# Kernel tuning notes

Hardware: AMD Instinct MI355X
Metric: run time of the kernel (lower is better)

Reference implementation:

```python
import jax, jax.numpy as jnp
import numpy as np

HEADS = 8
DIM_HEAD = 64
DIM_INNER = HEADS * DIM_HEAD  # 512
SCALE = DIM_HEAD ** -0.5
B, N, D = 8, 512, 512
NEG = -1e9


def setup_inputs() -> dict:
    key = jax.random.key(0)
    ks = jax.random.split(key, 12)
    inp = {}
    for i in range(3):
        inp[f"x{i}"] = jax.random.normal(ks[i], (B, N, D), dtype=jnp.float32)
        inp[f"m{i}"] = jax.random.randint(ks[3 + i], (B, N), 0, 2).astype(bool)
        inp[f"Wqkv{i}"] = jax.random.normal(ks[6 + i], (D, 3 * DIM_INNER), dtype=jnp.float32) * 0.02
        inp[f"Wout{i}"] = jax.random.normal(ks[9 + i], (DIM_INNER, D), dtype=jnp.float32) * 0.02
    return inp


def _split_heads(t):
    # [b, n, h*d] -> [b, h, n, d]
    b, n, _ = t.shape
    return t.reshape(b, n, HEADS, DIM_HEAD).transpose(0, 2, 1, 3)


def _forward(xs, masks, Wqkvs, Wouts):
    qs, ks, vs = [], [], []
    for x, W in zip(xs, Wqkvs):
        q, k, v = jnp.split(x @ W, 3, axis=-1)
        qs.append(_split_heads(q))
        ks.append(_split_heads(k))
        vs.append(_split_heads(v))
    K = jnp.concatenate(ks, axis=2)  # [b, h, 3n, d]
    V = jnp.concatenate(vs, axis=2)
    outs = []
    for q, m, Wo in zip(qs, masks, Wouts):
        dots = jnp.einsum('bhnd,bhmd->bhnm', q, K) * SCALE
        # original masks whole query rows: masked_fill(~mask[:, None, :, None], -1e9)
        dots = jnp.where(m[:, None, :, None], dots, NEG)
        attn = jax.nn.softmax(dots, axis=-1)  # dropout is identity at eval
        o = jnp.einsum('bhnm,bhmd->bhnd', attn, V)
        o = o.transpose(0, 2, 1, 3).reshape(q.shape[0], q.shape[2], DIM_INNER)
        outs.append(o @ Wo)
    return tuple(outs)


def reference(x0, x1, x2, m0, m1, m2, Wqkv0, Wqkv1, Wqkv2, Wout0, Wout1, Wout2):
    return _forward((x0, x1, x2), (m0, m1, m2), (Wqkv0, Wqkv1, Wqkv2), (Wout0, Wout1, Wout2))
```

## Files before the change

### kernel.cpp

```cpp
#include <hip/hip_runtime.h>
#include <cstdint>
#include <cstddef>

#define NEGV  -1.0e9f
#define QSCALE 0.18033688011112042f

typedef _Float16 h8 __attribute__((ext_vector_type(8)));
typedef _Float16 h4 __attribute__((ext_vector_type(4)));
typedef float    f4 __attribute__((ext_vector_type(4)));


__global__ __launch_bounds__(256) void cvt_x(
    const float* __restrict__ x0, const float* __restrict__ x1, const float* __restrict__ x2,
    _Float16* __restrict__ xh)
{
    const int mod = blockIdx.y;
    const float* __restrict__ s = (mod == 0) ? x0 : ((mod == 1) ? x1 : x2);
    _Float16* __restrict__ d = xh + (size_t)mod * 2097152;
    const int i = (blockIdx.x * 256 + threadIdx.x) * 4;
    float4 v = *reinterpret_cast<const float4*>(&s[i]);
    h4 o = { (_Float16)v.x, (_Float16)v.y, (_Float16)v.z, (_Float16)v.w };
    *reinterpret_cast<h4*>(&d[i]) = o;
}

__global__ __launch_bounds__(256) void tr_cvt(
    const float* __restrict__ s0, const float* __restrict__ s1, const float* __restrict__ s2,
    _Float16* __restrict__ dst, int R, int C)
{
    const int mod = blockIdx.z;
    const float* __restrict__ s = (mod == 0) ? s0 : ((mod == 1) ? s1 : s2);
    _Float16* __restrict__ d = dst + (size_t)mod * R * C;
    const int c0 = blockIdx.x * 32, r0 = blockIdx.y * 32;
    __shared__ float tile[32][33];
    const int tr = threadIdx.x >> 3;
    const int tc = (threadIdx.x & 7) * 4;
    float4 v = *reinterpret_cast<const float4*>(&s[(size_t)(r0 + tr) * C + c0 + tc]);
    tile[tr][tc + 0] = v.x; tile[tr][tc + 1] = v.y; tile[tr][tc + 2] = v.z; tile[tr][tc + 3] = v.w;
    __syncthreads();
    h4 o = { (_Float16)tile[tc + 0][tr], (_Float16)tile[tc + 1][tr],
             (_Float16)tile[tc + 2][tr], (_Float16)tile[tc + 3][tr] };
    *reinterpret_cast<h4*>(&d[(size_t)(c0 + tr) * R + r0 + tc]) = o;
}

__global__ __launch_bounds__(256) void qkv_gemm_f16(
    const _Float16* __restrict__ xh, const _Float16* __restrict__ Wqt,
    _Float16* __restrict__ Qh, _Float16* __restrict__ Kh, _Float16* __restrict__ Vt)
{
    const int mod = blockIdx.z;
    const _Float16* __restrict__ A  = xh  + (size_t)mod * 4096 * 512;
    const _Float16* __restrict__ Bw = Wqt + (size_t)mod * 1536 * 512;

    __shared__ _Float16 As[128 * 40];
    __shared__ _Float16 Bs[128 * 40];

    const int t = threadIdx.x;
    const int brow = blockIdx.y * 128, bcol = blockIdx.x * 128;
    const int w = t >> 6, l = t & 63;
    const int wr = (w >> 1) * 64, wc = (w & 1) * 64;
    const int lr = l & 15, lk = (l >> 4) * 8, lg = l >> 4;

    const int sm0 = t >> 2,        skk = (t & 3) * 8;
    const int sm1 = (t + 256) >> 2;

    f4 acc[4][4] = {};
    h8 arg[2], brg[2];

    arg[0] = *reinterpret_cast<const h8*>(&A [(size_t)(brow + sm0) * 512 + skk]);
    arg[1] = *reinterpret_cast<const h8*>(&A [(size_t)(brow + sm1) * 512 + skk]);
    brg[0] = *reinterpret_cast<const h8*>(&Bw[(size_t)(bcol + sm0) * 512 + skk]);
    brg[1] = *reinterpret_cast<const h8*>(&Bw[(size_t)(bcol + sm1) * 512 + skk]);
    *reinterpret_cast<h8*>(&As[sm0 * 40 + skk]) = arg[0];
    *reinterpret_cast<h8*>(&As[sm1 * 40 + skk]) = arg[1];
    *reinterpret_cast<h8*>(&Bs[sm0 * 40 + skk]) = brg[0];
    *reinterpret_cast<h8*>(&Bs[sm1 * 40 + skk]) = brg[1];

    for (int k0 = 0; k0 < 512; k0 += 32) {
        __syncthreads();
        const bool more = (k0 + 32) < 512;
        if (more) {
            const int kn = k0 + 32;
            arg[0] = *reinterpret_cast<const h8*>(&A [(size_t)(brow + sm0) * 512 + kn + skk]);
            arg[1] = *reinterpret_cast<const h8*>(&A [(size_t)(brow + sm1) * 512 + kn + skk]);
            brg[0] = *reinterpret_cast<const h8*>(&Bw[(size_t)(bcol + sm0) * 512 + kn + skk]);
            brg[1] = *reinterpret_cast<const h8*>(&Bw[(size_t)(bcol + sm1) * 512 + kn + skk]);
        }
        h8 af[4], bf[4];
#pragma unroll
        for (int m = 0; m < 4; m++)
            af[m] = *reinterpret_cast<h8*>(&As[(wr + m * 16 + lr) * 40 + lk]);
#pragma unroll
        for (int n = 0; n < 4; n++)
            bf[n] = *reinterpret_cast<h8*>(&Bs[(wc + n * 16 + lr) * 40 + lk]);
        __builtin_amdgcn_s_setprio(1);
#pragma unroll
        for (int m = 0; m < 4; m++)
#pragma unroll
            for (int n = 0; n < 4; n++)
                acc[m][n] = __builtin_amdgcn_mfma_f32_16x16x32_f16(af[m], bf[n], acc[m][n], 0, 0, 0);
        __builtin_amdgcn_s_setprio(0);
        __syncthreads();
        if (more) {
            *reinterpret_cast<h8*>(&As[sm0 * 40 + skk]) = arg[0];
            *reinterpret_cast<h8*>(&As[sm1 * 40 + skk]) = arg[1];
            *reinterpret_cast<h8*>(&Bs[sm0 * 40 + skk]) = brg[0];
            *reinterpret_cast<h8*>(&Bs[sm1 * 40 + skk]) = brg[1];
        }
    }

    const int sec = bcol >> 9;
    const int b = brow >> 9;
    const int nbase = brow & 511;
    const int cbase = bcol - (sec << 9);

#pragma unroll
    for (int m = 0; m < 4; m++) {
        const int rloc = wr + m * 16 + lg * 4;
#pragma unroll
        for (int reg = 0; reg < 4; reg++) {
            const int n = nbase + rloc + reg;
#pragma unroll
            for (int nn = 0; nn < 4; nn++) {
                const int cis = cbase + wc + nn * 16 + lr;
                const int h = cis >> 6, d = cis & 63;
                const float v = acc[m][nn][reg];
                if (sec == 0) {
                    Qh[((((size_t)mod * 8 + b) * 8 + h) * 512 + n) * 64 + d] = (_Float16)(v * QSCALE);
                } else if (sec == 1) {
                    Kh[(((size_t)b * 8 + h) * 1536 + mod * 512 + n) * 64 + d] = (_Float16)v;
                } else {
                    Vt[(((size_t)b * 8 + h) * 64 + d) * 1536 + mod * 512 + n] = (_Float16)v;
                }
            }
        }
    }
}

__global__ __launch_bounds__(256) void attn_f16(
    const _Float16* __restrict__ Qh, const _Float16* __restrict__ Kh, const _Float16* __restrict__ Vt,
    const int* __restrict__ m0, const int* __restrict__ m1, const int* __restrict__ m2,
    _Float16* __restrict__ Oh)
{
    const int mod = blockIdx.z;
    const int bh = blockIdx.y, b = bh >> 3, h = bh & 7;
    const int q0 = blockIdx.x * 64;

    __shared__ _Float16 Ks[64 * 72];
    __shared__ _Float16 Vs[64 * 72];
    __shared__ _Float16 Ps[64 * 72];

    const int t = threadIdx.x, w = t >> 6, l = t & 63;
    const int lr = l & 15, lg = l >> 4, lk = lg * 8;

    const _Float16* __restrict__ Qp = Qh + ((((size_t)mod * 8 + b) * 8 + h) * 512 + q0 + w * 16) * 64;
    h8 qf0 = *reinterpret_cast<const h8*>(&Qp[(size_t)lr * 64 + lk]);
    h8 qf1 = *reinterpret_cast<const h8*>(&Qp[(size_t)lr * 64 + 32 + lk]);

    const int* __restrict__ mk = (mod == 0) ? m0 : ((mod == 1) ? m1 : m2);
    const bool msk = mk[b * 512 + q0 + w * 16 + lr] != 0;

    float mrow = -3.0e38f, lsum = 0.f;
    f4 o[4] = {};

    const _Float16* __restrict__ Kp = Kh + (size_t)bh * 1536 * 64;
    const _Float16* __restrict__ Vp = Vt + (size_t)bh * 64 * 1536;

    const int sr0 = t >> 3,        skk = (t & 7) * 8;
    const int sr1 = (t + 256) >> 3;

    h8 krg[2], vrg[2];
    krg[0] = *reinterpret_cast<const h8*>(&Kp[(size_t)sr0 * 64 + skk]);
    krg[1] = *reinterpret_cast<const h8*>(&Kp[(size_t)sr1 * 64 + skk]);
    vrg[0] = *reinterpret_cast<const h8*>(&Vp[(size_t)sr0 * 1536 + skk]);
    vrg[1] = *reinterpret_cast<const h8*>(&Vp[(size_t)sr1 * 1536 + skk]);
    *reinterpret_cast<h8*>(&Ks[sr0 * 72 + skk]) = krg[0];
    *reinterpret_cast<h8*>(&Ks[sr1 * 72 + skk]) = krg[1];
    *reinterpret_cast<h8*>(&Vs[sr0 * 72 + skk]) = vrg[0];
    *reinterpret_cast<h8*>(&Vs[sr1 * 72 + skk]) = vrg[1];

    for (int c0 = 0; c0 < 1536; c0 += 64) {
        __syncthreads();
        const bool more = (c0 + 64) < 1536;
        if (more) {
            const int cn = c0 + 64;
            krg[0] = *reinterpret_cast<const h8*>(&Kp[(size_t)(cn + sr0) * 64 + skk]);
            krg[1] = *reinterpret_cast<const h8*>(&Kp[(size_t)(cn + sr1) * 64 + skk]);
            vrg[0] = *reinterpret_cast<const h8*>(&Vp[(size_t)sr0 * 1536 + cn + skk]);
            vrg[1] = *reinterpret_cast<const h8*>(&Vp[(size_t)sr1 * 1536 + cn + skk]);
        }

        f4 st[4] = {};
        __builtin_amdgcn_s_setprio(1);
#pragma unroll
        for (int kb = 0; kb < 4; kb++) {
            h8 ka0 = *reinterpret_cast<h8*>(&Ks[(kb * 16 + lr) * 72 + lk]);
            h8 ka1 = *reinterpret_cast<h8*>(&Ks[(kb * 16 + lr) * 72 + 32 + lk]);
            st[kb] = __builtin_amdgcn_mfma_f32_16x16x32_f16(ka0, qf0, st[kb], 0, 0, 0);
            st[kb] = __builtin_amdgcn_mfma_f32_16x16x32_f16(ka1, qf1, st[kb], 0, 0, 0);
        }
        __builtin_amdgcn_s_setprio(0);

        if (!msk) {
#pragma unroll
            for (int kb = 0; kb < 4; kb++) { st[kb][0] = NEGV; st[kb][1] = NEGV; st[kb][2] = NEGV; st[kb][3] = NEGV; }
        }
        float cm = fmaxf(fmaxf(fmaxf(st[0][0], st[0][1]), fmaxf(st[0][2], st[0][3])),
                         fmaxf(fmaxf(st[1][0], st[1][1]), fmaxf(st[1][2], st[1][3])));
        cm = fmaxf(cm, fmaxf(fmaxf(fmaxf(st[2][0], st[2][1]), fmaxf(st[2][2], st[2][3])),
                             fmaxf(fmaxf(st[3][0], st[3][1]), fmaxf(st[3][2], st[3][3]))));
        cm = fmaxf(cm, __shfl_xor(cm, 16));
        cm = fmaxf(cm, __shfl_xor(cm, 32));

        if (!__all(cm <= mrow + 8.0f)) {
            const float mn = fmaxf(mrow, cm);
            const float sc = __builtin_amdgcn_exp2f(mrow - mn);
            mrow = mn;
            lsum *= sc;
#pragma unroll
            for (int dg = 0; dg < 4; dg++) o[dg] *= sc;
        }

        float rs = 0.f;
#pragma unroll
        for (int kb = 0; kb < 4; kb++) {
            const float p0 = __builtin_amdgcn_exp2f(st[kb][0] - mrow);
            const float p1 = __builtin_amdgcn_exp2f(st[kb][1] - mrow);
            const float p2 = __builtin_amdgcn_exp2f(st[kb][2] - mrow);
            const float p3 = __builtin_amdgcn_exp2f(st[kb][3] - mrow);
            rs += (p0 + p1) + (p2 + p3);
            h4 ph = { (_Float16)p0, (_Float16)p1, (_Float16)p2, (_Float16)p3 };
            *reinterpret_cast<h4*>(&Ps[(w * 16 + lr) * 72 + kb * 16 + lg * 4]) = ph;
        }
        rs += __shfl_xor(rs, 16);
        rs += __shfl_xor(rs, 32);
        lsum += rs;

        __builtin_amdgcn_s_setprio(1);
#pragma unroll
        for (int kb2 = 0; kb2 < 2; kb2++) {
            h8 pa = *reinterpret_cast<h8*>(&Ps[(w * 16 + lr) * 72 + kb2 * 32 + lk]);
#pragma unroll
            for (int dg = 0; dg < 4; dg++) {
                h8 va = *reinterpret_cast<h8*>(&Vs[(dg * 16 + lr) * 72 + kb2 * 32 + lk]);
                o[dg] = __builtin_amdgcn_mfma_f32_16x16x32_f16(va, pa, o[dg], 0, 0, 0);
            }
        }
        __builtin_amdgcn_s_setprio(0);

        __syncthreads();
        if (more) {
            *reinterpret_cast<h8*>(&Ks[sr0 * 72 + skk]) = krg[0];
            *reinterpret_cast<h8*>(&Ks[sr1 * 72 + skk]) = krg[1];
            *reinterpret_cast<h8*>(&Vs[sr0 * 72 + skk]) = vrg[0];
            *reinterpret_cast<h8*>(&Vs[sr1 * 72 + skk]) = vrg[1];
        }
    }

    const float inv = 1.f / lsum;
    const size_t row = (size_t)mod * 4096 + b * 512 + q0 + w * 16 + lr;
#pragma unroll
    for (int dg = 0; dg < 4; dg++) {
        h4 ov = { (_Float16)(o[dg][0] * inv), (_Float16)(o[dg][1] * inv),
                  (_Float16)(o[dg][2] * inv), (_Float16)(o[dg][3] * inv) };
        *reinterpret_cast<h4*>(&Oh[row * 512 + h * 64 + dg * 16 + lg * 4]) = ov;
    }
}

__global__ __launch_bounds__(256) void out_gemm_f16(
    const _Float16* __restrict__ Oh, const _Float16* __restrict__ Wot,
    float* __restrict__ out)
{
    const int mod = blockIdx.z;
    const _Float16* __restrict__ A  = Oh  + (size_t)mod * 4096 * 512;
    const _Float16* __restrict__ Bw = Wot + (size_t)mod * 512 * 512;
    float* __restrict__ C = out + (size_t)mod * 4096 * 512;

    __shared__ _Float16 As[128 * 40];
    __shared__ _Float16 Bs[128 * 40];

    const int t = threadIdx.x;
    const int brow = blockIdx.y * 128, bcol = blockIdx.x * 128;
    const int w = t >> 6, l = t & 63;
    const int wr = (w >> 1) * 64, wc = (w & 1) * 64;
    const int lr = l & 15, lk = (l >> 4) * 8, lg = l >> 4;

    const int sm0 = t >> 2,        skk = (t & 3) * 8;
    const int sm1 = (t + 256) >> 2;

    f4 acc[4][4] = {};
    h8 arg[2], brg[2];

    arg[0] = *reinterpret_cast<const h8*>(&A [(size_t)(brow + sm0) * 512 + skk]);
    arg[1] = *reinterpret_cast<const h8*>(&A [(size_t)(brow + sm1) * 512 + skk]);
    brg[0] = *reinterpret_cast<const h8*>(&Bw[(size_t)(bcol + sm0) * 512 + skk]);
    brg[1] = *reinterpret_cast<const h8*>(&Bw[(size_t)(bcol + sm1) * 512 + skk]);
    *reinterpret_cast<h8*>(&As[sm0 * 40 + skk]) = arg[0];
    *reinterpret_cast<h8*>(&As[sm1 * 40 + skk]) = arg[1];
    *reinterpret_cast<h8*>(&Bs[sm0 * 40 + skk]) = brg[0];
    *reinterpret_cast<h8*>(&Bs[sm1 * 40 + skk]) = brg[1];

    for (int k0 = 0; k0 < 512; k0 += 32) {
        __syncthreads();
        const bool more = (k0 + 32) < 512;
        if (more) {
            const int kn = k0 + 32;
            arg[0] = *reinterpret_cast<const h8*>(&A [(size_t)(brow + sm0) * 512 + kn + skk]);
            arg[1] = *reinterpret_cast<const h8*>(&A [(size_t)(brow + sm1) * 512 + kn + skk]);
            brg[0] = *reinterpret_cast<const h8*>(&Bw[(size_t)(bcol + sm0) * 512 + kn + skk]);
            brg[1] = *reinterpret_cast<const h8*>(&Bw[(size_t)(bcol + sm1) * 512 + kn + skk]);
        }
        h8 af[4], bf[4];
#pragma unroll
        for (int m = 0; m < 4; m++)
            af[m] = *reinterpret_cast<h8*>(&As[(wr + m * 16 + lr) * 40 + lk]);
#pragma unroll
        for (int n = 0; n < 4; n++)
            bf[n] = *reinterpret_cast<h8*>(&Bs[(wc + n * 16 + lr) * 40 + lk]);
        __builtin_amdgcn_s_setprio(1);
#pragma unroll
        for (int m = 0; m < 4; m++)
#pragma unroll
            for (int n = 0; n < 4; n++)
                acc[m][n] = __builtin_amdgcn_mfma_f32_16x16x32_f16(af[m], bf[n], acc[m][n], 0, 0, 0);
        __builtin_amdgcn_s_setprio(0);
        __syncthreads();
        if (more) {
            *reinterpret_cast<h8*>(&As[sm0 * 40 + skk]) = arg[0];
            *reinterpret_cast<h8*>(&As[sm1 * 40 + skk]) = arg[1];
            *reinterpret_cast<h8*>(&Bs[sm0 * 40 + skk]) = brg[0];
            *reinterpret_cast<h8*>(&Bs[sm1 * 40 + skk]) = brg[1];
        }
    }

#pragma unroll
    for (int m = 0; m < 4; m++) {
        const int rloc = wr + m * 16 + lg * 4;
#pragma unroll
        for (int reg = 0; reg < 4; reg++) {
            const size_t base = (size_t)(brow + rloc + reg) * 512 + bcol;
#pragma unroll
            for (int nn = 0; nn < 4; nn++)
                C[base + wc + nn * 16 + lr] = acc[m][nn][reg];
        }
    }
}

extern "C" void kernel_launch(void* const* d_in, const int* in_sizes, int n_in,
                              void* d_out, int out_size, void* d_ws, size_t ws_size,
                              hipStream_t stream)
{
    const float* x0  = (const float*)d_in[0];
    const int*   m0  = (const int*)  d_in[1];
    const float* Wq0 = (const float*)d_in[2];
    const float* Wo0 = (const float*)d_in[3];
    const float* x1  = (const float*)d_in[4];
    const int*   m1  = (const int*)  d_in[5];
    const float* Wq1 = (const float*)d_in[6];
    const float* Wo1 = (const float*)d_in[7];
    const float* x2  = (const float*)d_in[8];
    const int*   m2  = (const int*)  d_in[9];
    const float* Wq2 = (const float*)d_in[10];
    const float* Wo2 = (const float*)d_in[11];

    _Float16* xh  = (_Float16*)d_ws;
    _Float16* Wqt = xh  + 6291456;
    _Float16* Wot = Wqt + 2359296;
    _Float16* Qh  = Wot + 786432;
    _Float16* Kh  = Qh  + 6291456;
    _Float16* Vt  = Kh  + 6291456;
    _Float16* Oh  = Vt  + 6291456;

    cvt_x <<<dim3(2048, 3), 256, 0, stream>>>(x0, x1, x2, xh);
    tr_cvt<<<dim3(48, 16, 3), 256, 0, stream>>>(Wq0, Wq1, Wq2, Wqt, 512, 1536);
    tr_cvt<<<dim3(16, 16, 3), 256, 0, stream>>>(Wo0, Wo1, Wo2, Wot, 512, 512);

    qkv_gemm_f16<<<dim3(12, 32, 3), 256, 0, stream>>>(xh, Wqt, Qh, Kh, Vt);
    attn_f16    <<<dim3(8, 64, 3), 256, 0, stream>>>(Qh, Kh, Vt, m0, m1, m2, Oh);
    out_gemm_f16<<<dim3(4, 32, 3), 256, 0, stream>>>(Oh, Wot, (float*)d_out);
}
```

Measured before the change: 266.6 us.

## Fuse x conversion into QKV GEMM, stage epilogue via LDS, enlarge attention blocks

Removes the separate fp32->fp16 conversion kernel for x and instead loads fp32 activations inside the QKV GEMM, converting them while staging into shared memory. The Q/K epilogue now goes through an LDS transpose tile so it can issue 16-byte vectorized stores, and V is written as 4-wide vectors instead of scalars. The attention kernel moves to 512-thread blocks covering 128 queries each, so every K/V chunk loaded into LDS serves twice as many query rows. Grid axes are swapped so that consecutive blocks share the same weight tile. The trade-offs are twice the fp32 global read traffic for A inside the GEMM and higher per-block resource use in attention.

```diff
diff --git a/kernel.cpp b/kernel.cpp
--- a/kernel.cpp
+++ b/kernel.cpp
@@ -10,17 +10,10 @@
 typedef float    f4 __attribute__((ext_vector_type(4)));
 
 
-__global__ __launch_bounds__(256) void cvt_x(
-    const float* __restrict__ x0, const float* __restrict__ x1, const float* __restrict__ x2,
-    _Float16* __restrict__ xh)
-{
-    const int mod = blockIdx.y;
-    const float* __restrict__ s = (mod == 0) ? x0 : ((mod == 1) ? x1 : x2);
-    _Float16* __restrict__ d = xh + (size_t)mod * 2097152;
-    const int i = (blockIdx.x * 256 + threadIdx.x) * 4;
-    float4 v = *reinterpret_cast<const float4*>(&s[i]);
-    h4 o = { (_Float16)v.x, (_Float16)v.y, (_Float16)v.z, (_Float16)v.w };
-    *reinterpret_cast<h4*>(&d[i]) = o;
+static __device__ inline h8 cvt8(float4 a, float4 b) {
+    h8 r = { (_Float16)a.x, (_Float16)a.y, (_Float16)a.z, (_Float16)a.w,
+             (_Float16)b.x, (_Float16)b.y, (_Float16)b.z, (_Float16)b.w };
+    return r;
 }
 
 __global__ __launch_bounds__(256) void tr_cvt(
@@ -43,24 +36,267 @@
 }
 
 __global__ __launch_bounds__(256) void qkv_gemm_f16(
-    const _Float16* __restrict__ xh, const _Float16* __restrict__ Wqt,
+    const float* __restrict__ x0, const float* __restrict__ x1, const float* __restrict__ x2,
+    const _Float16* __restrict__ Wqt,
     _Float16* __restrict__ Qh, _Float16* __restrict__ Kh, _Float16* __restrict__ Vt)
 {
     const int mod = blockIdx.z;
-    const _Float16* __restrict__ A  = xh  + (size_t)mod * 4096 * 512;
+    const float* __restrict__ A = (mod == 0) ? x0 : ((mod == 1) ? x1 : x2);
     const _Float16* __restrict__ Bw = Wqt + (size_t)mod * 1536 * 512;
 
-    __shared__ _Float16 As[128 * 40];
-    __shared__ _Float16 Bs[128 * 40];
+    __shared__ _Float16 smem[2 * 128 * 40];
+    _Float16* As = smem;
+    _Float16* Bs = smem + 128 * 40;
 
     const int t = threadIdx.x;
-    const int brow = blockIdx.y * 128, bcol = blockIdx.x * 128;
+    const int brow = blockIdx.x * 128, bcol = blockIdx.y * 128;
     const int w = t >> 6, l = t & 63;
     const int wr = (w >> 1) * 64, wc = (w & 1) * 64;
     const int lr = l & 15, lk = (l >> 4) * 8, lg = l >> 4;
 
-    const int sm0 = t >> 2,        skk = (t & 3) * 8;
-    const int sm1 = (t + 256) >> 2;
+    const int sm0 = t >> 2, skk = (t & 3) * 8, sm1 = sm0 + 64;
+
+    f4 acc[4][4] = {};
+    float4 axr[2][2];
+    h8 brg[2];
+
+    axr[0][0] = *reinterpret_cast<const float4*>(&A[(size_t)(brow + sm0) * 512 + skk]);
+    axr[0][1] = *reinterpret_cast<const float4*>(&A[(size_t)(brow + sm0) * 512 + skk + 4]);
+    axr[1][0] = *reinterpret_cast<const float4*>(&A[(size_t)(brow + sm1) * 512 + skk]);
+    axr[1][1] = *reinterpret_cast<const float4*>(&A[(size_t)(brow + sm1) * 512 + skk + 4]);
+    brg[0] = *reinterpret_cast<const h8*>(&Bw[(size_t)(bcol + sm0) * 512 + skk]);
+    brg[1] = *reinterpret_cast<const h8*>(&Bw[(size_t)(bcol + sm1) * 512 + skk]);
+    *reinterpret_cast<h8*>(&As[sm0 * 40 + skk]) = cvt8(axr[0][0], axr[0][1]);
+    *reinterpret_cast<h8*>(&As[sm1 * 40 + skk]) = cvt8(axr[1][0], axr[1][1]);
+    *reinterpret_cast<h8*>(&Bs[sm0 * 40 + skk]) = brg[0];
+    *reinterpret_cast<h8*>(&Bs[sm1 * 40 + skk]) = brg[1];
+
+    for (int k0 = 0; k0 < 512; k0 += 32) {
+        __syncthreads();
+        const bool more = (k0 + 32) < 512;
+        if (more) {
+            const int kn = k0 + 32 + skk;
+            axr[0][0] = *reinterpret_cast<const float4*>(&A[(size_t)(brow + sm0) * 512 + kn]);
+            axr[0][1] = *reinterpret_cast<const float4*>(&A[(size_t)(brow + sm0) * 512 + kn + 4]);
+            axr[1][0] = *reinterpret_cast<const float4*>(&A[(size_t)(brow + sm1) * 512 + kn]);
+            axr[1][1] = *reinterpret_cast<const float4*>(&A[(size_t)(brow + sm1) * 512 + kn + 4]);
+            brg[0] = *reinterpret_cast<const h8*>(&Bw[(size_t)(bcol + sm0) * 512 + k0 + 32 + skk]);
+            brg[1] = *reinterpret_cast<const h8*>(&Bw[(size_t)(bcol + sm1) * 512 + k0 + 32 + skk]);
+        }
+        h8 af[4], bf[4];
+#pragma unroll
+        for (int m = 0; m < 4; m++)
+            af[m] = *reinterpret_cast<h8*>(&As[(wr + m * 16 + lr) * 40 + lk]);
+#pragma unroll
+        for (int n = 0; n < 4; n++)
+            bf[n] = *reinterpret_cast<h8*>(&Bs[(wc + n * 16 + lr) * 40 + lk]);
+        __builtin_amdgcn_s_setprio(1);
+#pragma unroll
+        for (int m = 0; m < 4; m++)
+#pragma unroll
+            for (int n = 0; n < 4; n++)
+                acc[m][n] = __builtin_amdgcn_mfma_f32_16x16x32_f16(af[m], bf[n], acc[m][n], 0, 0, 0);
+        __builtin_amdgcn_s_setprio(0);
+        __syncthreads();
+        if (more) {
+            *reinterpret_cast<h8*>(&As[sm0 * 40 + skk]) = cvt8(axr[0][0], axr[0][1]);
+            *reinterpret_cast<h8*>(&As[sm1 * 40 + skk]) = cvt8(axr[1][0], axr[1][1]);
+            *reinterpret_cast<h8*>(&Bs[sm0 * 40 + skk]) = brg[0];
+            *reinterpret_cast<h8*>(&Bs[sm1 * 40 + skk]) = brg[1];
+        }
+    }
+
+    const int sec = bcol >> 9;
+    const int b = brow >> 9;
+    const int nbase = brow & 511;
+    const int cbase = bcol - (sec << 9);
+
+    if (sec == 2) {
+#pragma unroll
+        for (int m = 0; m < 4; m++) {
+            const int n = nbase + wr + m * 16 + lg * 4;
+#pragma unroll
+            for (int nn = 0; nn < 4; nn++) {
+                const int cis = cbase + wc + nn * 16 + lr;
+                const int hh = cis >> 6, d = cis & 63;
+                h4 pv = { (_Float16)acc[m][nn][0], (_Float16)acc[m][nn][1],
+                          (_Float16)acc[m][nn][2], (_Float16)acc[m][nn][3] };
+                *reinterpret_cast<h4*>(&Vt[(((size_t)b * 8 + hh) * 64 + d) * 1536 + mod * 512 + n]) = pv;
+            }
+        }
+    } else {
+        const float scl = (sec == 0) ? QSCALE : 1.0f;
+        _Float16 (*Ts)[136] = reinterpret_cast<_Float16(*)[136]>(smem);
+#pragma unroll
+        for (int pass = 0; pass < 2; pass++) {
+            __syncthreads();
+            if ((w >> 1) == pass) {
+#pragma unroll
+                for (int m = 0; m < 4; m++)
+#pragma unroll
+                    for (int nn = 0; nn < 4; nn++)
+#pragma unroll
+                        for (int reg = 0; reg < 4; reg++)
+                            Ts[m * 16 + lg * 4 + reg][wc + nn * 16 + lr] =
+                                (_Float16)(acc[m][nn][reg] * scl);
+            }
+            __syncthreads();
+#pragma unroll
+            for (int it = 0; it < 4; it++) {
+                const int idx = t + it * 256;
+                const int r = idx >> 4, c = (idx & 15) * 8;
+                h8 v = *reinterpret_cast<h8*>(&Ts[r][c]);
+                const int n = nbase + pass * 64 + r;
+                const int cis = cbase + c;
+                const int hh = cis >> 6, d = cis & 63;
+                if (sec == 0)
+                    *reinterpret_cast<h8*>(&Qh[((((size_t)mod * 8 + b) * 8 + hh) * 512 + n) * 64 + d]) = v;
+                else
+                    *reinterpret_cast<h8*>(&Kh[(((size_t)b * 8 + hh) * 1536 + mod * 512 + n) * 64 + d]) = v;
+            }
+        }
+    }
+}
+
+__global__ __launch_bounds__(512) void attn_f16(
+    const _Float16* __restrict__ Qh, const _Float16* __restrict__ Kh, const _Float16* __restrict__ Vt,
+    const int* __restrict__ m0, const int* __restrict__ m1, const int* __restrict__ m2,
+    _Float16* __restrict__ Oh)
+{
+    const int mod = blockIdx.z;
+    const int bh = blockIdx.x, b = bh >> 3, h = bh & 7;
+    const int q0 = blockIdx.y * 128;
+
+    __shared__ _Float16 Ks[64 * 72];
+    __shared__ _Float16 Vs[64 * 72];
+    __shared__ _Float16 Ps[128 * 72];
+
+    const int t = threadIdx.x, w = t >> 6, l = t & 63;
+    const int lr = l & 15, lg = l >> 4, lk = lg * 8;
+
+    const _Float16* __restrict__ Qp = Qh + ((((size_t)mod * 8 + b) * 8 + h) * 512 + q0 + w * 16) * 64;
+    h8 qf0 = *reinterpret_cast<const h8*>(&Qp[(size_t)lr * 64 + lk]);
+    h8 qf1 = *reinterpret_cast<const h8*>(&Qp[(size_t)lr * 64 + 32 + lk]);
+
+    const int* __restrict__ mk = (mod == 0) ? m0 : ((mod == 1) ? m1 : m2);
+    const bool msk = mk[b * 512 + q0 + w * 16 + lr] != 0;
+
+    float mrow = -3.0e38f, lsum = 0.f;
+    f4 o[4] = {};
+
+    const int sr = t >> 3, skk = (t & 7) * 8;
+    const _Float16* __restrict__ kSrc = Kh + (size_t)bh * 1536 * 64 + (size_t)sr * 64 + skk;
+    const _Float16* __restrict__ vSrc = Vt + (size_t)bh * 64 * 1536 + (size_t)sr * 1536 + skk;
+    _Float16* kDst = &Ks[sr * 72 + skk];
+    _Float16* vDst = &Vs[sr * 72 + skk];
+
+    h8 krg = *reinterpret_cast<const h8*>(kSrc);
+    h8 vrg = *reinterpret_cast<const h8*>(vSrc);
+    *reinterpret_cast<h8*>(kDst) = krg;
+    *reinterpret_cast<h8*>(vDst) = vrg;
+
+    for (int c0 = 0; c0 < 1536; c0 += 64) {
+        __syncthreads();
+        const bool more = (c0 + 64) < 1536;
+        if (more) {
+            krg = *reinterpret_cast<const h8*>(kSrc + (size_t)(c0 + 64) * 64);
+            vrg = *reinterpret_cast<const h8*>(vSrc + (c0 + 64));
+        }
+
+        f4 st[4] = {};
+        __builtin_amdgcn_s_setprio(1);
+#pragma unroll
+        for (int kb = 0; kb < 4; kb++) {
+            h8 ka0 = *reinterpret_cast<h8*>(&Ks[(kb * 16 + lr) * 72 + lk]);
+            h8 ka1 = *reinterpret_cast<h8*>(&Ks[(kb * 16 + lr) * 72 + 32 + lk]);
+            st[kb] = __builtin_amdgcn_mfma_f32_16x16x32_f16(ka0, qf0, st[kb], 0, 0, 0);
+            st[kb] = __builtin_amdgcn_mfma_f32_16x16x32_f16(ka1, qf1, st[kb], 0, 0, 0);
+        }
+        __builtin_amdgcn_s_setprio(0);
+
+        if (!msk) {
+#pragma unroll
+            for (int kb = 0; kb < 4; kb++) { st[kb][0] = NEGV; st[kb][1] = NEGV; st[kb][2] = NEGV; st[kb][3] = NEGV; }
+        }
+        float cm = fmaxf(fmaxf(fmaxf(st[0][0], st[0][1]), fmaxf(st[0][2], st[0][3])),
+                         fmaxf(fmaxf(st[1][0], st[1][1]), fmaxf(st[1][2], st[1][3])));
+        cm = fmaxf(cm, fmaxf(fmaxf(fmaxf(st[2][0], st[2][1]), fmaxf(st[2][2], st[2][3])),
+                             fmaxf(fmaxf(st[3][0], st[3][1]), fmaxf(st[3][2], st[3][3]))));
+        cm = fmaxf(cm, __shfl_xor(cm, 16));
+        cm = fmaxf(cm, __shfl_xor(cm, 32));
+
+        if (!__all(cm <= mrow + 8.0f)) {
+            const float mn = fmaxf(mrow, cm);
+            const float sc = __builtin_amdgcn_exp2f(mrow - mn);
+            mrow = mn;
+            lsum *= sc;
+#pragma unroll
+            for (int dg = 0; dg < 4; dg++) o[dg] *= sc;
+        }
+
+        float rs = 0.f;
+#pragma unroll
+        for (int kb = 0; kb < 4; kb++) {
+            const float p0 = __builtin_amdgcn_exp2f(st[kb][0] - mrow);
+            const float p1 = __builtin_amdgcn_exp2f(st[kb][1] - mrow);
+            const float p2 = __builtin_amdgcn_exp2f(st[kb][2] - mrow);
+            const float p3 = __builtin_amdgcn_exp2f(st[kb][3] - mrow);
+            rs += (p0 + p1) + (p2 + p3);
+            h4 ph = { (_Float16)p0, (_Float16)p1, (_Float16)p2, (_Float16)p3 };
+            *reinterpret_cast<h4*>(&Ps[(w * 16 + lr) * 72 + kb * 16 + lg * 4]) = ph;
+        }
+        rs += __shfl_xor(rs, 16);
+        rs += __shfl_xor(rs, 32);
+        lsum += rs;
+
+        __builtin_amdgcn_s_setprio(1);
+#pragma unroll
+        for (int kb2 = 0; kb2 < 2; kb2++) {
+            h8 pa = *reinterpret_cast<h8*>(&Ps[(w * 16 + lr) * 72 + kb2 * 32 + lk]);
+#pragma unroll
+            for (int dg = 0; dg < 4; dg++) {
+                h8 va = *reinterpret_cast<h8*>(&Vs[(dg * 16 + lr) * 72 + kb2 * 32 + lk]);
+                o[dg] = __builtin_amdgcn_mfma_f32_16x16x32_f16(va, pa, o[dg], 0, 0, 0);
+            }
+        }
+        __builtin_amdgcn_s_setprio(0);
+
+        __syncthreads();
+        if (more) {
+            *reinterpret_cast<h8*>(kDst) = krg;
+            *reinterpret_cast<h8*>(vDst) = vrg;
+        }
+    }
+
+    const float inv = 1.f / lsum;
+    const size_t row = (size_t)mod * 4096 + b * 512 + q0 + w * 16 + lr;
+#pragma unroll
+    for (int dg = 0; dg < 4; dg++) {
+        h4 ov = { (_Float16)(o[dg][0] * inv), (_Float16)(o[dg][1] * inv),
+                  (_Float16)(o[dg][2] * inv), (_Float16)(o[dg][3] * inv) };
+        *reinterpret_cast<h4*>(&Oh[row * 512 + h * 64 + dg * 16 + lg * 4]) = ov;
+    }
+}
+
+__global__ __launch_bounds__(256) void out_gemm_f16(
+    const _Float16* __restrict__ Oh, const _Float16* __restrict__ Wot,
+    float* __restrict__ out)
+{
+    const int mod = blockIdx.z;
+    const _Float16* __restrict__ A  = Oh  + (size_t)mod * 4096 * 512;
+    const _Float16* __restrict__ Bw = Wot + (size_t)mod * 512 * 512;
+    float* __restrict__ C = out + (size_t)mod * 4096 * 512;
+
+    __shared__ _Float16 As[128 * 40];
+    __shared__ _Float16 Bs[128 * 40];
+
+    const int t = threadIdx.x;
+    const int brow = blockIdx.x * 128, bcol = blockIdx.y * 128;
+    const int w = t >> 6, l = t & 63;
+    const int wr = (w >> 1) * 64, wc = (w & 1) * 64;
+    const int lr = l & 15, lk = (l >> 4) * 8, lg = l >> 4;
+
+    const int sm0 = t >> 2, skk = (t & 3) * 8, sm1 = sm0 + 64;
 
     f4 acc[4][4] = {};
     h8 arg[2], brg[2];
@@ -78,235 +314,11 @@
         __syncthreads();
         const bool more = (k0 + 32) < 512;
         if (more) {
-            const int kn = k0 + 32;
-            arg[0] = *reinterpret_cast<const h8*>(&A [(size_t)(brow + sm0) * 512 + kn + skk]);
-            arg[1] = *reinterpret_cast<const h8*>(&A [(size_t)(brow + sm1) * 512 + kn + skk]);
-            brg[0] = *reinterpret_cast<const h8*>(&Bw[(size_t)(bcol + sm0) * 512 + kn + skk]);
-            brg[1] = *reinterpret_cast<const h8*>(&Bw[(size_t)(bcol + sm1) * 512 + kn + skk]);
-        }
-        h8 af[4], bf[4];
-#pragma unroll
-        for (int m = 0; m < 4; m++)
-            af[m] = *reinterpret_cast<h8*>(&As[(wr + m * 16 + lr) * 40 + lk]);
-#pragma unroll
-        for (int n = 0; n < 4; n++)
-            bf[n] = *reinterpret_cast<h8*>(&Bs[(wc + n * 16 + lr) * 40 + lk]);
-        __builtin_amdgcn_s_setprio(1);
-#pragma unroll
-        for (int m = 0; m < 4; m++)
-#pragma unroll
-            for (int n = 0; n < 4; n++)
-                acc[m][n] = __builtin_amdgcn_mfma_f32_16x16x32_f16(af[m], bf[n], acc[m][n], 0, 0, 0);
-        __builtin_amdgcn_s_setprio(0);
-        __syncthreads();
-        if (more) {
-            *reinterpret_cast<h8*>(&As[sm0 * 40 + skk]) = arg[0];
-            *reinterpret_cast<h8*>(&As[sm1 * 40 + skk]) = arg[1];
-            *reinterpret_cast<h8*>(&Bs[sm0 * 40 + skk]) = brg[0];
-            *reinterpret_cast<h8*>(&Bs[sm1 * 40 + skk]) = brg[1];
-        }
-    }
-
-    const int sec = bcol >> 9;
-    const int b = brow >> 9;
-    const int nbase = brow & 511;
-    const int cbase = bcol - (sec << 9);
-
-#pragma unroll
-    for (int m = 0; m < 4; m++) {
-        const int rloc = wr + m * 16 + lg * 4;
-#pragma unroll
-        for (int reg = 0; reg < 4; reg++) {
-            const int n = nbase + rloc + reg;
-#pragma unroll
-            for (int nn = 0; nn < 4; nn++) {
-                const int cis = cbase + wc + nn * 16 + lr;
-                const int h = cis >> 6, d = cis & 63;
-                const float v = acc[m][nn][reg];
-                if (sec == 0) {
-                    Qh[((((size_t)mod * 8 + b) * 8 + h) * 512 + n) * 64 + d] = (_Float16)(v * QSCALE);
-                } else if (sec == 1) {
-                    Kh[(((size_t)b * 8 + h) * 1536 + mod * 512 + n) * 64 + d] = (_Float16)v;
-                } else {
-                    Vt[(((size_t)b * 8 + h) * 64 + d) * 1536 + mod * 512 + n] = (_Float16)v;
-                }
-            }
-        }
-    }
-}
-
-__global__ __launch_bounds__(256) void attn_f16(
-    const _Float16* __restrict__ Qh, const _Float16* __restrict__ Kh, const _Float16* __restrict__ Vt,
-    const int* __restrict__ m0, const int* __restrict__ m1, const int* __restrict__ m2,
-    _Float16* __restrict__ Oh)
-{
-    const int mod = blockIdx.z;
-    const int bh = blockIdx.y, b = bh >> 3, h = bh & 7;
-    const int q0 = blockIdx.x * 64;
-
-    __shared__ _Float16 Ks[64 * 72];
-    __shared__ _Float16 Vs[64 * 72];
-    __shared__ _Float16 Ps[64 * 72];
-
-    const int t = threadIdx.x, w = t >> 6, l = t & 63;
-    const int lr = l & 15, lg = l >> 4, lk = lg * 8;
-
-    const _Float16* __restrict__ Qp = Qh + ((((size_t)mod * 8 + b) * 8 + h) * 512 + q0 + w * 16) * 64;
-    h8 qf0 = *reinterpret_cast<const h8*>(&Qp[(size_t)lr * 64 + lk]);
-    h8 qf1 = *reinterpret_cast<const h8*>(&Qp[(size_t)lr * 64 + 32 + lk]);
-
-    const int* __restrict__ mk = (mod == 0) ? m0 : ((mod == 1) ? m1 : m2);
-    const bool msk = mk[b * 512 + q0 + w * 16 + lr] != 0;
-
-    float mrow = -3.0e38f, lsum = 0.f;
-    f4 o[4] = {};
-
-    const _Float16* __restrict__ Kp = Kh + (size_t)bh * 1536 * 64;
-    const _Float16* __restrict__ Vp = Vt + (size_t)bh * 64 * 1536;
-
-    const int sr0 = t >> 3,        skk = (t & 7) * 8;
-    const int sr1 = (t + 256) >> 3;
-
-    h8 krg[2], vrg[2];
-    krg[0] = *reinterpret_cast<const h8*>(&Kp[(size_t)sr0 * 64 + skk]);
-    krg[1] = *reinterpret_cast<const h8*>(&Kp[(size_t)sr1 * 64 + skk]);
-    vrg[0] = *reinterpret_cast<const h8*>(&Vp[(size_t)sr0 * 1536 + skk]);
-    vrg[1] = *reinterpret_cast<const h8*>(&Vp[(size_t)sr1 * 1536 + skk]);
-    *reinterpret_cast<h8*>(&Ks[sr0 * 72 + skk]) = krg[0];
-    *reinterpret_cast<h8*>(&Ks[sr1 * 72 + skk]) = krg[1];
-    *reinterpret_cast<h8*>(&Vs[sr0 * 72 + skk]) = vrg[0];
-    *reinterpret_cast<h8*>(&Vs[sr1 * 72 + skk]) = vrg[1];
-
-    for (int c0 = 0; c0 < 1536; c0 += 64) {
-        __syncthreads();
-        const bool more = (c0 + 64) < 1536;
-        if (more) {
-            const int cn = c0 + 64;
-            krg[0] = *reinterpret_cast<const h8*>(&Kp[(size_t)(cn + sr0) * 64 + skk]);
-            krg[1] = *reinterpret_cast<const h8*>(&Kp[(size_t)(cn + sr1) * 64 + skk]);
-            vrg[0] = *reinterpret_cast<const h8*>(&Vp[(size_t)sr0 * 1536 + cn + skk]);
-            vrg[1] = *reinterpret_cast<const h8*>(&Vp[(size_t)sr1 * 1536 + cn + skk]);
-        }
-
-        f4 st[4] = {};
-        __builtin_amdgcn_s_setprio(1);
-#pragma unroll
-        for (int kb = 0; kb < 4; kb++) {
-            h8 ka0 = *reinterpret_cast<h8*>(&Ks[(kb * 16 + lr) * 72 + lk]);
-            h8 ka1 = *reinterpret_cast<h8*>(&Ks[(kb * 16 + lr) * 72 + 32 + lk]);
-            st[kb] = __builtin_amdgcn_mfma_f32_16x16x32_f16(ka0, qf0, st[kb], 0, 0, 0);
-            st[kb] = __builtin_amdgcn_mfma_f32_16x16x32_f16(ka1, qf1, st[kb], 0, 0, 0);
-        }
-        __builtin_amdgcn_s_setprio(0);
-
-        if (!msk) {
-#pragma unroll
-            for (int kb = 0; kb < 4; kb++) { st[kb][0] = NEGV; st[kb][1] = NEGV; st[kb][2] = NEGV; st[kb][3] = NEGV; }
-        }
-        float cm = fmaxf(fmaxf(fmaxf(st[0][0], st[0][1]), fmaxf(st[0][2], st[0][3])),
-                         fmaxf(fmaxf(st[1][0], st[1][1]), fmaxf(st[1][2], st[1][3])));
-        cm = fmaxf(cm, fmaxf(fmaxf(fmaxf(st[2][0], st[2][1]), fmaxf(st[2][2], st[2][3])),
-                             fmaxf(fmaxf(st[3][0], st[3][1]), fmaxf(st[3][2], st[3][3]))));
-        cm = fmaxf(cm, __shfl_xor(cm, 16));
-        cm = fmaxf(cm, __shfl_xor(cm, 32));
-
-        if (!__all(cm <= mrow + 8.0f)) {
-            const float mn = fmaxf(mrow, cm);
-            const float sc = __builtin_amdgcn_exp2f(mrow - mn);
-            mrow = mn;
-            lsum *= sc;
-#pragma unroll
-            for (int dg = 0; dg < 4; dg++) o[dg] *= sc;
-        }
-
-        float rs = 0.f;
-#pragma unroll
-        for (int kb = 0; kb < 4; kb++) {
-            const float p0 = __builtin_amdgcn_exp2f(st[kb][0] - mrow);
-            const float p1 = __builtin_amdgcn_exp2f(st[kb][1] - mrow);
-            const float p2 = __builtin_amdgcn_exp2f(st[kb][2] - mrow);
-            const float p3 = __builtin_amdgcn_exp2f(st[kb][3] - mrow);
-            rs += (p0 + p1) + (p2 + p3);
-            h4 ph = { (_Float16)p0, (_Float16)p1, (_Float16)p2, (_Float16)p3 };
-            *reinterpret_cast<h4*>(&Ps[(w * 16 + lr) * 72 + kb * 16 + lg * 4]) = ph;
-        }
-        rs += __shfl_xor(rs, 16);
-        rs += __shfl_xor(rs, 32);
-        lsum += rs;
-
-        __builtin_amdgcn_s_setprio(1);
-#pragma unroll
-        for (int kb2 = 0; kb2 < 2; kb2++) {
-            h8 pa = *reinterpret_cast<h8*>(&Ps[(w * 16 + lr) * 72 + kb2 * 32 + lk]);
-#pragma unroll
-            for (int dg = 0; dg < 4; dg++) {
-                h8 va = *reinterpret_cast<h8*>(&Vs[(dg * 16 + lr) * 72 + kb2 * 32 + lk]);
-                o[dg] = __builtin_amdgcn_mfma_f32_16x16x32_f16(va, pa, o[dg], 0, 0, 0);
-            }
-        }
-        __builtin_amdgcn_s_setprio(0);
-
-        __syncthreads();
-        if (more) {
-            *reinterpret_cast<h8*>(&Ks[sr0 * 72 + skk]) = krg[0];
-            *reinterpret_cast<h8*>(&Ks[sr1 * 72 + skk]) = krg[1];
-            *reinterpret_cast<h8*>(&Vs[sr0 * 72 + skk]) = vrg[0];
-            *reinterpret_cast<h8*>(&Vs[sr1 * 72 + skk]) = vrg[1];
-        }
-    }
-
-    const float inv = 1.f / lsum;
-    const size_t row = (size_t)mod * 4096 + b * 512 + q0 + w * 16 + lr;
-#pragma unroll
-    for (int dg = 0; dg < 4; dg++) {
-        h4 ov = { (_Float16)(o[dg][0] * inv), (_Float16)(o[dg][1] * inv),
-                  (_Float16)(o[dg][2] * inv), (_Float16)(o[dg][3] * inv) };
-        *reinterpret_cast<h4*>(&Oh[row * 512 + h * 64 + dg * 16 + lg * 4]) = ov;
-    }
-}
-
-__global__ __launch_bounds__(256) void out_gemm_f16(
-    const _Float16* __restrict__ Oh, const _Float16* __restrict__ Wot,
-    float* __restrict__ out)
-{
-    const int mod = blockIdx.z;
-    const _Float16* __restrict__ A  = Oh  + (size_t)mod * 4096 * 512;
-    const _Float16* __restrict__ Bw = Wot + (size_t)mod * 512 * 512;
-    float* __restrict__ C = out + (size_t)mod * 4096 * 512;
-
-    __shared__ _Float16 As[128 * 40];
-    __shared__ _Float16 Bs[128 * 40];
-
-    const int t = threadIdx.x;
-    const int brow = blockIdx.y * 128, bcol = blockIdx.x * 128;
-    const int w = t >> 6, l = t & 63;
-    const int wr = (w >> 1) * 64, wc = (w & 1) * 64;
-    const int lr = l & 15, lk = (l >> 4) * 8, lg = l >> 4;
-
-    const int sm0 = t >> 2,        skk = (t & 3) * 8;
-    const int sm1 = (t + 256) >> 2;
-
-    f4 acc[4][4] = {};
-    h8 arg[2], brg[2];
-
-    arg[0] = *reinterpret_cast<const h8*>(&A [(size_t)(brow + sm0) * 512 + skk]);
-    arg[1] = *reinterpret_cast<const h8*>(&A [(size_t)(brow + sm1) * 512 + skk]);
-    brg[0] = *reinterpret_cast<const h8*>(&Bw[(size_t)(bcol + sm0) * 512 + skk]);
-    brg[1] = *reinterpret_cast<const h8*>(&Bw[(size_t)(bcol + sm1) * 512 + skk]);
-    *reinterpret_cast<h8*>(&As[sm0 * 40 + skk]) = arg[0];
-    *reinterpret_cast<h8*>(&As[sm1 * 40 + skk]) = arg[1];
-    *reinterpret_cast<h8*>(&Bs[sm0 * 40 + skk]) = brg[0];
-    *reinterpret_cast<h8*>(&Bs[sm1 * 40 + skk]) = brg[1];
-
-    for (int k0 = 0; k0 < 512; k0 += 32) {
-        __syncthreads();
-        const bool more = (k0 + 32) < 512;
-        if (more) {
-            const int kn = k0 + 32;
-            arg[0] = *reinterpret_cast<const h8*>(&A [(size_t)(brow + sm0) * 512 + kn + skk]);
-            arg[1] = *reinterpret_cast<const h8*>(&A [(size_t)(brow + sm1) * 512 + kn + skk]);
-            brg[0] = *reinterpret_cast<const h8*>(&Bw[(size_t)(bcol + sm0) * 512 + kn + skk]);
-            brg[1] = *reinterpret_cast<const h8*>(&Bw[(size_t)(bcol + sm1) * 512 + kn + skk]);
+            const int kn = k0 + 32 + skk;
+            arg[0] = *reinterpret_cast<const h8*>(&A [(size_t)(brow + sm0) * 512 + kn]);
+            arg[1] = *reinterpret_cast<const h8*>(&A [(size_t)(brow + sm1) * 512 + kn]);
+            brg[0] = *reinterpret_cast<const h8*>(&Bw[(size_t)(bcol + sm0) * 512 + kn]);
+            brg[1] = *reinterpret_cast<const h8*>(&Bw[(size_t)(bcol + sm1) * 512 + kn]);
         }
         h8 af[4], bf[4];
 #pragma unroll
@@ -361,19 +373,17 @@
     const float* Wq2 = (const float*)d_in[10];
     const float* Wo2 = (const float*)d_in[11];
 
-    _Float16* xh  = (_Float16*)d_ws;
-    _Float16* Wqt = xh  + 6291456;
+    _Float16* Wqt = (_Float16*)d_ws;
     _Float16* Wot = Wqt + 2359296;
     _Float16* Qh  = Wot + 786432;
     _Float16* Kh  = Qh  + 6291456;
     _Float16* Vt  = Kh  + 6291456;
     _Float16* Oh  = Vt  + 6291456;
 
-    cvt_x <<<dim3(2048, 3), 256, 0, stream>>>(x0, x1, x2, xh);
     tr_cvt<<<dim3(48, 16, 3), 256, 0, stream>>>(Wq0, Wq1, Wq2, Wqt, 512, 1536);
     tr_cvt<<<dim3(16, 16, 3), 256, 0, stream>>>(Wo0, Wo1, Wo2, Wot, 512, 512);
 
-    qkv_gemm_f16<<<dim3(12, 32, 3), 256, 0, stream>>>(xh, Wqt, Qh, Kh, Vt);
-    attn_f16    <<<dim3(8, 64, 3), 256, 0, stream>>>(Qh, Kh, Vt, m0, m1, m2, Oh);
-    out_gemm_f16<<<dim3(4, 32, 3), 256, 0, stream>>>(Oh, Wot, (float*)d_out);
-}
+    qkv_gemm_f16<<<dim3(32, 12, 3), 256, 0, stream>>>(x0, x1, x2, Wqt, Qh, Kh, Vt);
+    attn_f16    <<<dim3(64, 4, 3), 512, 0, stream>>>(Qh, Kh, Vt, m0, m1, m2, Oh);
+    out_gemm_f16<<<dim3(32, 4, 3), 256, 0, stream>>>(Oh, Wot, (float*)d_out);
+}
```

Result: faster. 230.7 us (-13.5%).
